# Kernel tuning notes

Measured on AMD Instinct MI355X. Metric: run time of the kernel, lower is better.

## Reference

```python
import jax, jax.numpy as jnp
import numpy as np
from jax.ops import segment_sum

N_NODES = 100000


def _deg_inv_sqrt(idx, n):
    # DGL GraphConv norm='both': degs clamped to min 1, then deg^{-0.5}
    deg = segment_sum(jnp.ones_like(idx, dtype=jnp.float32), idx, num_segments=n)
    return jnp.where(deg > 0, jax.lax.rsqrt(jnp.maximum(deg, 1.0)), 1.0)


def _graph_conv(x, src, dst, W, b, out_norm, in_norm, n):
    # norm='both': scale src feats by out_deg^-1/2, sum-aggregate, scale by in_deg^-1/2
    h = (x * out_norm[:, None]) @ W          # apply weight first (cheaper/equal width)
    msg = h[src]                              # [E, d] irregular gather
    agg = segment_sum(msg, dst, num_segments=n)
    return agg * in_norm[:, None] + b


def setup_inputs() -> dict:
    key = jax.random.key(0)
    k1, k2, k3, k4, k5, k6, k7 = jax.random.split(key, 7)
    E = 1600000
    in_feats, h_feats, out_feats = 128, 128, 64
    in_feat = jax.random.normal(k1, (N_NODES, in_feats), dtype=jnp.float32)
    src = jax.random.randint(k2, (E,), 0, N_NODES, dtype=jnp.int32)
    dst = jax.random.randint(k3, (E,), 0, N_NODES, dtype=jnp.int32)
    # Glorot-style init like dgl GraphConv
    W1 = jax.random.normal(k4, (in_feats, h_feats), dtype=jnp.float32) * (1.0 / np.sqrt(in_feats))
    b1 = jnp.zeros((h_feats,), dtype=jnp.float32)
    W2 = jax.random.normal(k5, (h_feats, out_feats), dtype=jnp.float32) * (1.0 / np.sqrt(h_feats))
    b2 = jnp.zeros((out_feats,), dtype=jnp.float32)
    return {"in_feat": in_feat, "src": src, "dst": dst, "W1": W1, "b1": b1, "W2": W2, "b2": b2}


def reference(in_feat, src, dst, W1, b1, W2, b2):
    n = in_feat.shape[0]
    out_norm = _deg_inv_sqrt(src, n)  # out-degree norm (source side)
    in_norm = _deg_inv_sqrt(dst, n)   # in-degree norm (destination side)
    h = _graph_conv(in_feat, src, dst, W1, b1, out_norm, in_norm, n)
    z = jax.nn.relu(h)
    h2 = _graph_conv(z, src, dst, W2, b2, out_norm, in_norm, n)
    return (h2, z)
```

## Files before the change

### kernel.cpp

```cpp
#include <hip/hip_runtime.h>

#define N_NODES 100000
#define N_EDGES 1600000
#define NB 391
#define BCAP 5120
#define PART_BLOCKS 250
#define EPB 6400

typedef __attribute__((ext_vector_type(8))) short short8;
typedef __attribute__((ext_vector_type(4))) float f32x4;

__device__ inline unsigned short f2bf(float f) {
    unsigned int u = __builtin_bit_cast(unsigned int, f);
    u += 0x7fffu + ((u >> 16) & 1u);
    return (unsigned short)(u >> 16);
}
__device__ inline float bf2f(unsigned short h) {
    unsigned int u = ((unsigned int)h) << 16;
    return __builtin_bit_cast(float, u);
}

__global__ __launch_bounds__(256) void k_xb(const float* __restrict__ x, const float* __restrict__ out_norm,
                                            unsigned short* __restrict__ xb) {
    int tid = blockIdx.x * 256 + threadIdx.x;
    int row = tid >> 5;
    float4 v = ((const float4*)x)[tid];
    float w = out_norm[row];
    unsigned int lo = (unsigned int)f2bf(v.x * w) | ((unsigned int)f2bf(v.y * w) << 16);
    unsigned int hi = (unsigned int)f2bf(v.z * w) | ((unsigned int)f2bf(v.w * w) << 16);
    ((uint2*)xb)[tid] = make_uint2(lo, hi);
}

__global__ __launch_bounds__(256) void k_pack_w(const float* __restrict__ W1, const float* __restrict__ W2,
                                                unsigned short* __restrict__ Wp1, unsigned short* __restrict__ Wp2) {
    int i = blockIdx.x * 256 + threadIdx.x;
    if (i < 2048) {
        int kq = i >> 7, c = i & 127;
#pragma unroll
        for (int j = 0; j < 8; j++) Wp1[i * 8 + j] = f2bf(W1[(kq * 8 + j) * 128 + c]);
    } else if (i < 3072) {
        int i2 = i - 2048;
        int kq = i2 >> 6, c = i2 & 63;
#pragma unroll
        for (int j = 0; j < 8; j++) Wp2[i2 * 8 + j] = f2bf(W2[(kq * 8 + j) * 64 + c]);
    }
}

__global__ __launch_bounds__(256) void k_part(const int* __restrict__ src, const int* __restrict__ dst,
                                              int* __restrict__ gcurD, int* __restrict__ gcurS,
                                              unsigned int* __restrict__ ebuf,
                                              unsigned char* __restrict__ ebufS) {
    __shared__ int histD[NB], gbaseD[NB];
    __shared__ int histS[NB], gbaseS[NB];
    for (int i = threadIdx.x; i < NB; i += 256) { histD[i] = 0; histS[i] = 0; }
    __syncthreads();
    int base = blockIdx.x * EPB;
    for (int i = threadIdx.x; i < EPB; i += 256) {
        int d = dst[base + i], s = src[base + i];
        atomicAdd(&histD[d >> 8], 1);
        atomicAdd(&histS[s >> 8], 1);
    }
    __syncthreads();
    for (int i = threadIdx.x; i < NB; i += 256) {
        gbaseD[i] = atomicAdd(&gcurD[i], histD[i]);
        gbaseS[i] = atomicAdd(&gcurS[i], histS[i]);
        histD[i] = 0;
        histS[i] = 0;
    }
    __syncthreads();
    for (int i = threadIdx.x; i < EPB; i += 256) {
        int d = dst[base + i], s = src[base + i];
        int bd = d >> 8;
        int r = atomicAdd(&histD[bd], 1);
        int pos = gbaseD[bd] + r;
        if (pos < BCAP) ebuf[(size_t)bd * BCAP + pos] = ((unsigned int)s << 8) | (unsigned int)(d & 255);
        int bs = s >> 8;
        int r2 = atomicAdd(&histS[bs], 1);
        int pos2 = gbaseS[bs] + r2;
        if (pos2 < BCAP) ebufS[(size_t)bs * BCAP + pos2] = (unsigned char)(s & 255);
    }
}

__global__ __launch_bounds__(256) void k_bhist(const unsigned char* __restrict__ ebufS,
                                               const int* __restrict__ gcurS,
                                               float* __restrict__ out_norm) {
    __shared__ int hist[256];
    int b = blockIdx.x, t = threadIdx.x;
    hist[t] = 0;
    __syncthreads();
    int ne = min(gcurS[b], BCAP);
    const unsigned char* eb = ebufS + (size_t)b * BCAP;
    for (int i = t; i < ne; i += 256) atomicAdd(&hist[eb[i]], 1);
    __syncthreads();
    int node = b * 256 + t;
    if (node < N_NODES) out_norm[node] = hist[t] > 0 ? rsqrtf((float)hist[t]) : 1.0f;
}

__global__ __launch_bounds__(512) void k_bscan(const int* __restrict__ gcurD, int* __restrict__ bbase,
                                               int* __restrict__ row_ptr) {
    __shared__ int s[NB + 1];
    int t = threadIdx.x;
    if (t < NB) s[t] = min(gcurD[t], BCAP);
    __syncthreads();
    if (t == 0) {
        int run = 0;
        for (int b = 0; b < NB; b++) { int v = s[b]; s[b] = run; run += v; }
        s[NB] = run;
    }
    __syncthreads();
    if (t < NB) bbase[t] = s[t];
    if (t == 0) { bbase[NB] = s[NB]; row_ptr[N_NODES] = s[NB]; }
}

__global__ __launch_bounds__(256) void k_bsort(const unsigned int* __restrict__ ebuf, const int* __restrict__ gcurD,
                                               const int* __restrict__ bbase, int* __restrict__ csr_src,
                                               int* __restrict__ row_ptr, float* __restrict__ in_norm) {
    __shared__ unsigned int st[BCAP];
    __shared__ int perm[BCAP];
    __shared__ int hist[256], cursor[256], sa[256], sb[256];
    int b = blockIdx.x, t = threadIdx.x;
    int ne = min(gcurD[b], BCAP);
    const unsigned int* eb = ebuf + (size_t)b * BCAP;
    hist[t] = 0;
    __syncthreads();
    for (int i = t; i < ne; i += 256) {
        unsigned int pk = eb[i];
        st[i] = pk;
        atomicAdd(&hist[pk & 255u], 1);
    }
    __syncthreads();
    sa[t] = hist[t];
    __syncthreads();
    int* cur = sa; int* nxt = sb;
    for (int o = 1; o < 256; o <<= 1) {
        int v = cur[t] + (t >= o ? cur[t - o] : 0);
        nxt[t] = v;
        __syncthreads();
        int* tmp = cur; cur = nxt; nxt = tmp;
    }
    int ex = cur[t] - hist[t];
    cursor[t] = ex;
    int node = b * 256 + t;
    if (node < N_NODES) {
        row_ptr[node] = bbase[b] + ex;
        in_norm[node] = hist[t] > 0 ? rsqrtf((float)hist[t]) : 1.0f;
    }
    __syncthreads();
    for (int i = t; i < ne; i += 256) {
        unsigned int pk = st[i];
        int pos = atomicAdd(&cursor[pk & 255u], 1);
        perm[pos] = (int)(pk >> 8);
    }
    __syncthreads();
    int gb = bbase[b];
    for (int i = t; i < ne; i += 256) csr_src[gb + i] = perm[i];
}

__global__ __launch_bounds__(256) void k_agg1(const unsigned short* __restrict__ xb,
                                              const int* __restrict__ row_ptr, const int* __restrict__ csr,
                                              const float* __restrict__ in_norm,
                                              unsigned short* __restrict__ aggb) {
    int wave = threadIdx.x >> 6, lane = threadIdx.x & 63;
    int d = blockIdx.x * 4 + wave;
    if (d >= N_NODES) return;
    int e0 = __builtin_amdgcn_readfirstlane(row_ptr[d]);
    int e1 = __builtin_amdgcn_readfirstlane(row_ptr[d + 1]);
    int col = lane << 1;
    float accL[8], accH[8];
#pragma unroll
    for (int j = 0; j < 8; j++) { accL[j] = 0.f; accH[j] = 0.f; }
    int e = e0;
    for (; e + 16 <= e1; e += 16) {
        int sI[16];
#pragma unroll
        for (int j = 0; j < 16; j++) sI[j] = __builtin_amdgcn_readfirstlane(csr[e + j]);
        unsigned int v[16];
#pragma unroll
        for (int j = 0; j < 16; j++) v[j] = *(const unsigned int*)(xb + (size_t)sI[j] * 128 + col);
#pragma unroll
        for (int j = 0; j < 16; j++) {
            accL[j & 7] += bf2f((unsigned short)(v[j] & 0xffffu));
            accH[j & 7] += bf2f((unsigned short)(v[j] >> 16));
        }
    }
    for (; e + 8 <= e1; e += 8) {
        int sI[8];
#pragma unroll
        for (int j = 0; j < 8; j++) sI[j] = __builtin_amdgcn_readfirstlane(csr[e + j]);
        unsigned int v[8];
#pragma unroll
        for (int j = 0; j < 8; j++) v[j] = *(const unsigned int*)(xb + (size_t)sI[j] * 128 + col);
#pragma unroll
        for (int j = 0; j < 8; j++) {
            accL[j] += bf2f((unsigned short)(v[j] & 0xffffu));
            accH[j] += bf2f((unsigned short)(v[j] >> 16));
        }
    }
    for (; e < e1; e++) {
        int s = __builtin_amdgcn_readfirstlane(csr[e]);
        unsigned int v = *(const unsigned int*)(xb + (size_t)s * 128 + col);
        accL[0] += bf2f((unsigned short)(v & 0xffffu));
        accH[0] += bf2f((unsigned short)(v >> 16));
    }
    float a0 = 0.f, a1 = 0.f;
#pragma unroll
    for (int j = 0; j < 8; j++) { a0 += accL[j]; a1 += accH[j]; }
    float w = in_norm[d];
    unsigned int pk = (unsigned int)f2bf(a0 * w) | ((unsigned int)f2bf(a1 * w) << 16);
    *(unsigned int*)(aggb + (size_t)d * 128 + col) = pk;
}

__global__ __launch_bounds__(256) void k_gemm12(const unsigned short* __restrict__ Ab,
                                                const unsigned short* __restrict__ Wp1,
                                                const unsigned short* __restrict__ Wp2,
                                                const float* __restrict__ bias1,
                                                const float* __restrict__ out_norm,
                                                float* __restrict__ z_out,
                                                unsigned short* __restrict__ tb) {
    __shared__ __align__(16) unsigned short lds1[16 * 128 * 8];
    __shared__ __align__(16) unsigned short lds2[16 * 64 * 8];
    __shared__ __align__(16) unsigned short zt[64 * 132];
    {
        const uint4* s1 = (const uint4*)Wp1; uint4* d1 = (uint4*)lds1;
        for (int i = threadIdx.x; i < 2048; i += 256) d1[i] = s1[i];
        const uint4* s2 = (const uint4*)Wp2; uint4* d2 = (uint4*)lds2;
        for (int i = threadIdx.x; i < 1024; i += 256) d2[i] = s2[i];
    }
    __syncthreads();
    int wave = threadIdx.x >> 6, lane = threadIdx.x & 63;
    int base = (blockIdx.x * 4 + wave) * 16;
    if (base >= N_NODES) return;
    int m = lane & 15, q = lane >> 4;
    short8 a[4];
#pragma unroll
    for (int t = 0; t < 4; t++) a[t] = *(const short8*)(Ab + (size_t)(base + m) * 128 + t * 32 + q * 8);
    f32x4 acc[8];
#pragma unroll
    for (int c = 0; c < 8; c++) acc[c] = (f32x4)(0.f);
#pragma unroll
    for (int ct = 0; ct < 8; ct++) {
#pragma unroll
        for (int t = 0; t < 4; t++) {
            short8 b = *(const short8*)(lds1 + ((t * 4 + q) * 128 + ct * 16 + m) * 8);
            acc[ct] = __builtin_amdgcn_mfma_f32_16x16x32_bf16(a[t], b, acc[ct], 0, 0, 0);
        }
    }
    float onr[4];
#pragma unroll
    for (int i = 0; i < 4; i++) onr[i] = out_norm[base + q * 4 + i];
#pragma unroll
    for (int ct = 0; ct < 8; ct++) {
        int col = ct * 16 + m;
        float bv = bias1[col];
#pragma unroll
        for (int i = 0; i < 4; i++) {
            int row = base + q * 4 + i;
            float v = acc[ct][i] + bv;
            v = v > 0.f ? v : 0.f;
            z_out[(size_t)row * 128 + col] = v;
            zt[(wave * 16 + q * 4 + i) * 132 + col] = f2bf(v * onr[i]);
        }
    }
    short8 a2[4];
#pragma unroll
    for (int t = 0; t < 4; t++) a2[t] = *(const short8*)(zt + (wave * 16 + m) * 132 + t * 32 + q * 8);
    f32x4 acc2[4];
#pragma unroll
    for (int c = 0; c < 4; c++) acc2[c] = (f32x4)(0.f);
#pragma unroll
    for (int ct = 0; ct < 4; ct++) {
#pragma unroll
        for (int t = 0; t < 4; t++) {
            short8 b = *(const short8*)(lds2 + ((t * 4 + q) * 64 + ct * 16 + m) * 8);
            acc2[ct] = __builtin_amdgcn_mfma_f32_16x16x32_bf16(a2[t], b, acc2[ct], 0, 0, 0);
        }
    }
#pragma unroll
    for (int ct = 0; ct < 4; ct++) {
        int col = ct * 16 + m;
#pragma unroll
        for (int i = 0; i < 4; i++) {
            int row = base + q * 4 + i;
            tb[(size_t)row * 64 + col] = f2bf(acc2[ct][i]);
        }
    }
}

__global__ __launch_bounds__(256) void k_agg2(const unsigned short* __restrict__ tb,
                                              const int* __restrict__ row_ptr, const int* __restrict__ csr,
                                              const float* __restrict__ in_norm, const float* __restrict__ b2,
                                              float* __restrict__ out_h2) {
    int wave = threadIdx.x >> 6, lane = threadIdx.x & 63;
    int d = blockIdx.x * 4 + wave;
    if (d >= N_NODES) return;
    int e0 = __builtin_amdgcn_readfirstlane(row_ptr[d]);
    int e1 = __builtin_amdgcn_readfirstlane(row_ptr[d + 1]);
    float acc[8];
#pragma unroll
    for (int j = 0; j < 8; j++) acc[j] = 0.f;
    int e = e0;
    for (; e + 16 <= e1; e += 16) {
        int sI[16];
#pragma unroll
        for (int j = 0; j < 16; j++) sI[j] = __builtin_amdgcn_readfirstlane(csr[e + j]);
        unsigned short v[16];
#pragma unroll
        for (int j = 0; j < 16; j++) v[j] = tb[(size_t)sI[j] * 64 + lane];
#pragma unroll
        for (int j = 0; j < 16; j++) acc[j & 7] += bf2f(v[j]);
    }
    for (; e + 8 <= e1; e += 8) {
        int sI[8];
#pragma unroll
        for (int j = 0; j < 8; j++) sI[j] = __builtin_amdgcn_readfirstlane(csr[e + j]);
        unsigned short v[8];
#pragma unroll
        for (int j = 0; j < 8; j++) v[j] = tb[(size_t)sI[j] * 64 + lane];
#pragma unroll
        for (int j = 0; j < 8; j++) acc[j] += bf2f(v[j]);
    }
    for (; e < e1; e++) {
        int s = __builtin_amdgcn_readfirstlane(csr[e]);
        acc[0] += bf2f(tb[(size_t)s * 64 + lane]);
    }
    float a = 0.f;
#pragma unroll
    for (int j = 0; j < 8; j++) a += acc[j];
    out_h2[(size_t)d * 64 + lane] = a * in_norm[d] + b2[lane];
}

extern "C" void kernel_launch(void* const* d_in, const int* in_sizes, int n_in,
                              void* d_out, int out_size, void* d_ws, size_t ws_size,
                              hipStream_t stream) {
    const float* x   = (const float*)d_in[0];
    const int*   src = (const int*)d_in[1];
    const int*   dst = (const int*)d_in[2];
    const float* W1  = (const float*)d_in[3];
    const float* b1  = (const float*)d_in[4];
    const float* W2  = (const float*)d_in[5];
    const float* b2  = (const float*)d_in[6];
    float* out_h2 = (float*)d_out;
    float* out_z  = (float*)d_out + N_NODES * 64;

    char* ws = (char*)d_ws;
    size_t off = 0;
    auto alloc = [&](size_t bytes) -> char* {
        char* p = ws + off;
        off = (off + bytes + 255) & ~(size_t)255;
        return p;
    };
    int* gcurD    = (int*)alloc(NB * 4);
    int* gcurS    = (int*)alloc(NB * 4);
    int* bbase    = (int*)alloc((NB + 1) * 4);
    int* row_ptr  = (int*)alloc((N_NODES + 1) * 4);
    float* out_norm = (float*)alloc(N_NODES * 4);
    float* in_norm  = (float*)alloc(N_NODES * 4);
    unsigned int* ebuf = (unsigned int*)alloc((size_t)NB * BCAP * 4);
    unsigned char* ebufS = (unsigned char*)alloc((size_t)NB * BCAP);
    int* csr_src  = (int*)alloc((size_t)N_EDGES * 4);
    unsigned short* Wp1 = (unsigned short*)alloc(2048 * 8 * 2);
    unsigned short* Wp2 = (unsigned short*)alloc(1024 * 8 * 2);
    unsigned short* xb    = (unsigned short*)alloc((size_t)N_NODES * 128 * 2);
    unsigned short* agg1b = (unsigned short*)alloc((size_t)N_NODES * 128 * 2);
    unsigned short* tb    = (unsigned short*)alloc((size_t)N_NODES * 64 * 2);
    (void)ws_size; (void)in_sizes; (void)n_in; (void)out_size;

    hipMemsetAsync(gcurD, 0, NB * 4, stream);
    hipMemsetAsync(gcurS, 0, NB * 4, stream);

    const int GD_AGG = (N_NODES + 3) / 4;
    const int GD_GEMM = (N_NODES / 16 + 3) / 4;

    k_part<<<PART_BLOCKS, 256, 0, stream>>>(src, dst, gcurD, gcurS, ebuf, ebufS);
    k_bhist<<<NB, 256, 0, stream>>>(ebufS, gcurS, out_norm);
    k_bscan<<<1, 512, 0, stream>>>(gcurD, bbase, row_ptr);
    k_bsort<<<NB, 256, 0, stream>>>(ebuf, gcurD, bbase, csr_src, row_ptr, in_norm);
    k_xb<<<N_NODES * 32 / 256, 256, 0, stream>>>(x, out_norm, xb);
    k_pack_w<<<12, 256, 0, stream>>>(W1, W2, Wp1, Wp2);
    k_agg1<<<GD_AGG, 256, 0, stream>>>(xb, row_ptr, csr_src, in_norm, agg1b);
    k_gemm12<<<GD_GEMM, 256, 0, stream>>>(agg1b, Wp1, Wp2, b1, out_norm, out_z, tb);
    k_agg2<<<GD_AGG, 256, 0, stream>>>(tb, row_ptr, csr_src, in_norm, b2, out_h2);
}
```

Measured before the change: 327.2 us.

## Slice edges by source range so all waves gather from the same window in lockstep

The edge sort now also buckets each destination's edges into 13 source-id slices, building a per-node 16-entry row pointer table. The aggregation kernels use a fixed grid of 8192 persistent waves, each owning 13 nodes. They sweep the slices in order so that, at a given time, all waves gather from roughly the same 8K-node source window, which is meant to improve L2 hit rate on the irregular gathers. The cost is losing the 16-wide unrolled gather batching (now one load per iteration, less memory-level parallelism), a 16x larger row-pointer table, and a more complex sort.

```diff
diff --git a/kernel.cpp b/kernel.cpp
--- a/kernel.cpp
+++ b/kernel.cpp
@@ -6,6 +6,9 @@
 #define BCAP 5120
 #define PART_BLOCKS 250
 #define EPB 6400
+#define NSLICE 13
+#define SLICE_SHIFT 13
+#define NWAVES 8192
 
 typedef __attribute__((ext_vector_type(8))) short short8;
 typedef __attribute__((ext_vector_type(4))) float f32x4;
@@ -96,8 +99,7 @@
     if (node < N_NODES) out_norm[node] = hist[t] > 0 ? rsqrtf((float)hist[t]) : 1.0f;
 }
 
-__global__ __launch_bounds__(512) void k_bscan(const int* __restrict__ gcurD, int* __restrict__ bbase,
-                                               int* __restrict__ row_ptr) {
+__global__ __launch_bounds__(512) void k_bscan(const int* __restrict__ gcurD, int* __restrict__ bbase) {
     __shared__ int s[NB + 1];
     int t = threadIdx.x;
     if (t < NB) s[t] = min(gcurD[t], BCAP);
@@ -109,27 +111,32 @@
     }
     __syncthreads();
     if (t < NB) bbase[t] = s[t];
-    if (t == 0) { bbase[NB] = s[NB]; row_ptr[N_NODES] = s[NB]; }
+    if (t == 0) bbase[NB] = s[NB];
 }
 
 __global__ __launch_bounds__(256) void k_bsort(const unsigned int* __restrict__ ebuf, const int* __restrict__ gcurD,
                                                const int* __restrict__ bbase, int* __restrict__ csr_src,
-                                               int* __restrict__ row_ptr, float* __restrict__ in_norm) {
+                                               int* __restrict__ rp2, float* __restrict__ in_norm) {
     __shared__ unsigned int st[BCAP];
     __shared__ int perm[BCAP];
-    __shared__ int hist[256], cursor[256], sa[256], sb[256];
+    __shared__ int hist[256 * 17];
+    __shared__ int sa[256], sb[256];
     int b = blockIdx.x, t = threadIdx.x;
     int ne = min(gcurD[b], BCAP);
     const unsigned int* eb = ebuf + (size_t)b * BCAP;
-    hist[t] = 0;
+    for (int i = t; i < 256 * 17; i += 256) hist[i] = 0;
     __syncthreads();
     for (int i = t; i < ne; i += 256) {
         unsigned int pk = eb[i];
         st[i] = pk;
-        atomicAdd(&hist[pk & 255u], 1);
-    }
-    __syncthreads();
-    sa[t] = hist[t];
+        int key = (int)(pk & 255u) * 17 + (int)(pk >> (8 + SLICE_SHIFT));
+        atomicAdd(&hist[key], 1);
+    }
+    __syncthreads();
+    int tot = 0;
+#pragma unroll
+    for (int k = 0; k < NSLICE; k++) tot += hist[t * 17 + k];
+    sa[t] = tot;
     __syncthreads();
     int* cur = sa; int* nxt = sb;
     for (int o = 1; o < 256; o <<= 1) {
@@ -138,76 +145,72 @@
         __syncthreads();
         int* tmp = cur; cur = nxt; nxt = tmp;
     }
-    int ex = cur[t] - hist[t];
-    cursor[t] = ex;
+    int nodeBase = cur[t] - tot;
+    int gb = bbase[b];
     int node = b * 256 + t;
     if (node < N_NODES) {
-        row_ptr[node] = bbase[b] + ex;
-        in_norm[node] = hist[t] > 0 ? rsqrtf((float)hist[t]) : 1.0f;
+        int run = gb + nodeBase;
+#pragma unroll
+        for (int k = 0; k < NSLICE; k++) {
+            rp2[(size_t)node * 16 + k] = run;
+            int c = hist[t * 17 + k];
+            hist[t * 17 + k] = run - gb;
+            run += c;
+        }
+        rp2[(size_t)node * 16 + 13] = run;
+        rp2[(size_t)node * 16 + 14] = run;
+        rp2[(size_t)node * 16 + 15] = run;
+        in_norm[node] = tot > 0 ? rsqrtf((float)tot) : 1.0f;
     }
     __syncthreads();
     for (int i = t; i < ne; i += 256) {
         unsigned int pk = st[i];
-        int pos = atomicAdd(&cursor[pk & 255u], 1);
+        int key = (int)(pk & 255u) * 17 + (int)(pk >> (8 + SLICE_SHIFT));
+        int pos = atomicAdd(&hist[key], 1);
         perm[pos] = (int)(pk >> 8);
     }
     __syncthreads();
-    int gb = bbase[b];
     for (int i = t; i < ne; i += 256) csr_src[gb + i] = perm[i];
 }
 
-__global__ __launch_bounds__(256) void k_agg1(const unsigned short* __restrict__ xb,
-                                              const int* __restrict__ row_ptr, const int* __restrict__ csr,
-                                              const float* __restrict__ in_norm,
-                                              unsigned short* __restrict__ aggb) {
-    int wave = threadIdx.x >> 6, lane = threadIdx.x & 63;
-    int d = blockIdx.x * 4 + wave;
-    if (d >= N_NODES) return;
-    int e0 = __builtin_amdgcn_readfirstlane(row_ptr[d]);
-    int e1 = __builtin_amdgcn_readfirstlane(row_ptr[d + 1]);
+__global__ __launch_bounds__(256, 8) void k_agg1(const unsigned short* __restrict__ xb,
+                                                 const int* __restrict__ rp2, const int* __restrict__ csr,
+                                                 const float* __restrict__ in_norm,
+                                                 unsigned short* __restrict__ aggb) {
+    int wave = __builtin_amdgcn_readfirstlane(threadIdx.x >> 6);
+    int lane = threadIdx.x & 63;
+    int wid = blockIdx.x * 4 + wave;
     int col = lane << 1;
-    float accL[8], accH[8];
-#pragma unroll
-    for (int j = 0; j < 8; j++) { accL[j] = 0.f; accH[j] = 0.f; }
-    int e = e0;
-    for (; e + 16 <= e1; e += 16) {
-        int sI[16];
-#pragma unroll
-        for (int j = 0; j < 16; j++) sI[j] = __builtin_amdgcn_readfirstlane(csr[e + j]);
-        unsigned int v[16];
-#pragma unroll
-        for (int j = 0; j < 16; j++) v[j] = *(const unsigned int*)(xb + (size_t)sI[j] * 128 + col);
-#pragma unroll
-        for (int j = 0; j < 16; j++) {
-            accL[j & 7] += bf2f((unsigned short)(v[j] & 0xffffu));
-            accH[j & 7] += bf2f((unsigned short)(v[j] >> 16));
-        }
-    }
-    for (; e + 8 <= e1; e += 8) {
-        int sI[8];
-#pragma unroll
-        for (int j = 0; j < 8; j++) sI[j] = __builtin_amdgcn_readfirstlane(csr[e + j]);
-        unsigned int v[8];
-#pragma unroll
-        for (int j = 0; j < 8; j++) v[j] = *(const unsigned int*)(xb + (size_t)sI[j] * 128 + col);
-#pragma unroll
-        for (int j = 0; j < 8; j++) {
-            accL[j] += bf2f((unsigned short)(v[j] & 0xffffu));
-            accH[j] += bf2f((unsigned short)(v[j] >> 16));
-        }
-    }
-    for (; e < e1; e++) {
-        int s = __builtin_amdgcn_readfirstlane(csr[e]);
-        unsigned int v = *(const unsigned int*)(xb + (size_t)s * 128 + col);
-        accL[0] += bf2f((unsigned short)(v & 0xffffu));
-        accH[0] += bf2f((unsigned short)(v >> 16));
-    }
-    float a0 = 0.f, a1 = 0.f;
-#pragma unroll
-    for (int j = 0; j < 8; j++) { a0 += accL[j]; a1 += accH[j]; }
-    float w = in_norm[d];
-    unsigned int pk = (unsigned int)f2bf(a0 * w) | ((unsigned int)f2bf(a1 * w) << 16);
-    *(unsigned int*)(aggb + (size_t)d * 128 + col) = pk;
+    float aL[13], aH[13];
+#pragma unroll
+    for (int k = 0; k < 13; k++) { aL[k] = 0.f; aH[k] = 0.f; }
+#pragma unroll 1
+    for (int p = 0; p < NSLICE; p++) {
+#pragma unroll
+        for (int k = 0; k < 13; k++) {
+            int d = wid + k * NWAVES;
+            if (d < N_NODES) {
+                int e0 = __builtin_amdgcn_readfirstlane(rp2[(size_t)d * 16 + p]);
+                int e1 = __builtin_amdgcn_readfirstlane(rp2[(size_t)d * 16 + p + 1]);
+#pragma unroll 1
+                for (int e = e0; e < e1; e++) {
+                    int s = __builtin_amdgcn_readfirstlane(csr[e]);
+                    unsigned int v = *(const unsigned int*)(xb + (size_t)s * 128 + col);
+                    aH[k] += __builtin_bit_cast(float, v & 0xffff0000u);
+                    aL[k] += __builtin_bit_cast(float, v << 16);
+                }
+            }
+        }
+    }
+#pragma unroll
+    for (int k = 0; k < 13; k++) {
+        int d = wid + k * NWAVES;
+        if (d < N_NODES) {
+            float w = in_norm[d];
+            unsigned int pk = (unsigned int)f2bf(aL[k] * w) | ((unsigned int)f2bf(aH[k] * w) << 16);
+            *(unsigned int*)(aggb + (size_t)d * 128 + col) = pk;
+        }
+    }
 }
 
 __global__ __launch_bounds__(256) void k_gemm12(const unsigned short* __restrict__ Ab,
@@ -286,47 +289,39 @@
     }
 }
 
-__global__ __launch_bounds__(256) void k_agg2(const unsigned short* __restrict__ tb,
-                                              const int* __restrict__ row_ptr, const int* __restrict__ csr,
-                                              const float* __restrict__ in_norm, const float* __restrict__ b2,
-                                              float* __restrict__ out_h2) {
-    int wave = threadIdx.x >> 6, lane = threadIdx.x & 63;
-    int d = blockIdx.x * 4 + wave;
-    if (d >= N_NODES) return;
-    int e0 = __builtin_amdgcn_readfirstlane(row_ptr[d]);
-    int e1 = __builtin_amdgcn_readfirstlane(row_ptr[d + 1]);
-    float acc[8];
-#pragma unroll
-    for (int j = 0; j < 8; j++) acc[j] = 0.f;
-    int e = e0;
-    for (; e + 16 <= e1; e += 16) {
-        int sI[16];
-#pragma unroll
-        for (int j = 0; j < 16; j++) sI[j] = __builtin_amdgcn_readfirstlane(csr[e + j]);
-        unsigned short v[16];
-#pragma unroll
-        for (int j = 0; j < 16; j++) v[j] = tb[(size_t)sI[j] * 64 + lane];
-#pragma unroll
-        for (int j = 0; j < 16; j++) acc[j & 7] += bf2f(v[j]);
-    }
-    for (; e + 8 <= e1; e += 8) {
-        int sI[8];
-#pragma unroll
-        for (int j = 0; j < 8; j++) sI[j] = __builtin_amdgcn_readfirstlane(csr[e + j]);
-        unsigned short v[8];
-#pragma unroll
-        for (int j = 0; j < 8; j++) v[j] = tb[(size_t)sI[j] * 64 + lane];
-#pragma unroll
-        for (int j = 0; j < 8; j++) acc[j] += bf2f(v[j]);
-    }
-    for (; e < e1; e++) {
-        int s = __builtin_amdgcn_readfirstlane(csr[e]);
-        acc[0] += bf2f(tb[(size_t)s * 64 + lane]);
-    }
-    float a = 0.f;
-#pragma unroll
-    for (int j = 0; j < 8; j++) a += acc[j];
-    out_h2[(size_t)d * 64 + lane] = a * in_norm[d] + b2[lane];
+__global__ __launch_bounds__(256, 8) void k_agg2(const unsigned short* __restrict__ tb,
+                                                 const int* __restrict__ rp2, const int* __restrict__ csr,
+                                                 const float* __restrict__ in_norm, const float* __restrict__ b2,
+                                                 float* __restrict__ out_h2) {
+    int wave = __builtin_amdgcn_readfirstlane(threadIdx.x >> 6);
+    int lane = threadIdx.x & 63;
+    int wid = blockIdx.x * 4 + wave;
+    float bv = b2[lane];
+    float acc[13];
+#pragma unroll
+    for (int k = 0; k < 13; k++) acc[k] = 0.f;
+#pragma unroll 1
+    for (int p = 0; p < NSLICE; p++) {
+#pragma unroll
+        for (int k = 0; k < 13; k++) {
+            int d = wid + k * NWAVES;
+            if (d < N_NODES) {
+                int e0 = __builtin_amdgcn_readfirstlane(rp2[(size_t)d * 16 + p]);
+                int e1 = __builtin_amdgcn_readfirstlane(rp2[(size_t)d * 16 + p + 1]);
+#pragma unroll 1
+                for (int e = e0; e < e1; e++) {
+                    int s = __builtin_amdgcn_readfirstlane(csr[e]);
+                    unsigned int u = (unsigned int)tb[(size_t)s * 64 + lane];
+                    acc[k] += __builtin_bit_cast(float, u << 16);
+                }
+            }
+        }
+    }
+#pragma unroll
+    for (int k = 0; k < 13; k++) {
+        int d = wid + k * NWAVES;
+        if (d < N_NODES) out_h2[(size_t)d * 64 + lane] = acc[k] * in_norm[d] + bv;
+    }
 }
 
 extern "C" void kernel_launch(void* const* d_in, const int* in_sizes, int n_in,
@@ -352,7 +347,7 @@
     int* gcurD    = (int*)alloc(NB * 4);
     int* gcurS    = (int*)alloc(NB * 4);
     int* bbase    = (int*)alloc((NB + 1) * 4);
-    int* row_ptr  = (int*)alloc((N_NODES + 1) * 4);
+    int* rp2      = (int*)alloc((size_t)N_NODES * 16 * 4);
     float* out_norm = (float*)alloc(N_NODES * 4);
     float* in_norm  = (float*)alloc(N_NODES * 4);
     unsigned int* ebuf = (unsigned int*)alloc((size_t)NB * BCAP * 4);
@@ -368,16 +363,16 @@
     hipMemsetAsync(gcurD, 0, NB * 4, stream);
     hipMemsetAsync(gcurS, 0, NB * 4, stream);
 
-    const int GD_AGG = (N_NODES + 3) / 4;
+    const int GD_AGG = NWAVES / 4;
     const int GD_GEMM = (N_NODES / 16 + 3) / 4;
 
     k_part<<<PART_BLOCKS, 256, 0, stream>>>(src, dst, gcurD, gcurS, ebuf, ebufS);
     k_bhist<<<NB, 256, 0, stream>>>(ebufS, gcurS, out_norm);
-    k_bscan<<<1, 512, 0, stream>>>(gcurD, bbase, row_ptr);
-    k_bsort<<<NB, 256, 0, stream>>>(ebuf, gcurD, bbase, csr_src, row_ptr, in_norm);
+    k_bscan<<<1, 512, 0, stream>>>(gcurD, bbase);
+    k_bsort<<<NB, 256, 0, stream>>>(ebuf, gcurD, bbase, csr_src, rp2, in_norm);
     k_xb<<<N_NODES * 32 / 256, 256, 0, stream>>>(x, out_norm, xb);
     k_pack_w<<<12, 256, 0, stream>>>(W1, W2, Wp1, Wp2);
-    k_agg1<<<GD_AGG, 256, 0, stream>>>(xb, row_ptr, csr_src, in_norm, agg1b);
+    k_agg1<<<GD_AGG, 256, 0, stream>>>(xb, rp2, csr_src, in_norm, agg1b);
     k_gemm12<<<GD_GEMM, 256, 0, stream>>>(agg1b, Wp1, Wp2, b1, out_norm, out_z, tb);
-    k_agg2<<<GD_AGG, 256, 0, stream>>>(tb, row_ptr, csr_src, in_norm, b2, out_h2);
-}
+    k_agg2<<<GD_AGG, 256, 0, stream>>>(tb, rp2, csr_src, in_norm, b2, out_h2);
+}
```

New measurement: 487.0 us. 1.49x slower.
